# Kernel tuning notes

Measured on AMD Instinct MI355X. Metric: run time of the kernel, lower is better.

Reference implementation:

```python
import jax, jax.numpy as jnp
import numpy as np


def _gcn_norm(edge_index, num_nodes):
    # GCNConv default: add self-loops, symmetric normalization D^-1/2 (A+I) D^-1/2
    src, dst = edge_index[0], edge_index[1]
    loop = jnp.arange(num_nodes, dtype=edge_index.dtype)
    src = jnp.concatenate([src, loop])
    dst = jnp.concatenate([dst, loop])
    deg = jax.ops.segment_sum(jnp.ones_like(dst, dtype=jnp.float32), dst,
                              num_segments=num_nodes)
    dinv = jnp.where(deg > 0, jax.lax.rsqrt(deg), 0.0)
    norm = dinv[src] * dinv[dst]  # [E + N]
    return src, dst, norm


def _gcn_conv(x, W, b, src, dst, norm, num_nodes):
    # x: [B, N, Fin] -> [B, N, Fout]
    h = jnp.einsum('bnf,fh->bnh', x, W)
    msg = h[:, src, :] * norm[None, :, None]  # [B, E+N, Fout]
    agg = jax.vmap(lambda m: jax.ops.segment_sum(m, dst, num_segments=num_nodes))(msg)
    return agg + b


def setup_inputs() -> dict:
    key = jax.random.key(0)
    ks = jax.random.split(key, 10)
    B, N, E = 2, 20000, 320000
    Fin, H, Out = 128, 256, 1
    x = jax.random.normal(ks[0], (B, N, Fin), dtype=jnp.float32)
    edge_index = jax.random.randint(ks[1], (2, E), 0, N, dtype=jnp.int32)
    def lin(k, fan_in, shape):
        return jax.random.normal(k, shape, dtype=jnp.float32) / np.sqrt(fan_in)
    return {
        'x': x,
        'edge_index': edge_index,
        'W1': lin(ks[2], Fin, (Fin, H)), 'b1': jnp.zeros((H,), jnp.float32),
        'W2': lin(ks[3], H, (H, H)),     'b2': jnp.zeros((H,), jnp.float32),
        'W3': lin(ks[4], H, (H, H)),     'b3': jnp.zeros((H,), jnp.float32),
        'Wl': lin(ks[5], H, (H, Out)),   'bl': jnp.zeros((Out,), jnp.float32),
    }


def reference(x, edge_index, W1, b1, W2, b2, W3, b3, Wl, bl):
    N = x.shape[1]
    src, dst, norm = _gcn_norm(edge_index, N)
    h = jax.nn.relu(_gcn_conv(x, W1, b1, src, dst, norm, N))
    h = jax.nn.relu(_gcn_conv(h, W2, b2, src, dst, norm, N))
    h = jax.nn.relu(_gcn_conv(h, W3, b3, src, dst, norm, N))
    # AdaptiveAvgPool1d(1) over nodes -> mean over N, then linear head
    g = jnp.mean(h, axis=1)  # [B, H]
    return g @ Wl + bl  # [B, Out]
```

## Files before the change

kernel.cpp:

```cpp
#include <hip/hip_runtime.h>
#include <hip/hip_bf16.h>
#include <type_traits>

#define NN 20000
#define NE 320000
#define HD 256
#define NB 2
#define FIN 128
#define MP 40064
#define SB 79

typedef __attribute__((ext_vector_type(8))) short bf16x8;
typedef __attribute__((ext_vector_type(4))) float f32x4;

__device__ inline float bf2f(ushort u) {
    union { unsigned int i; float f; } c; c.i = ((unsigned int)u) << 16; return c.f;
}
__device__ inline ushort f2bf(float f) {
    __hip_bfloat16 h = __float2bfloat16(f);
    return *reinterpret_cast<ushort*>(&h);
}

__global__ __launch_bounds__(256) void count_kernel(const int* __restrict__ dst, int* cnt) {
    int e = blockIdx.x * 256 + threadIdx.x;
    if (e < NE) atomicAdd(&cnt[dst[e]], 1);
}

__global__ __launch_bounds__(256) void scan_blk_kernel(const int* __restrict__ cnt,
                                                       int* __restrict__ bsum,
                                                       float* __restrict__ dinv) {
    __shared__ int s[256];
    int t = threadIdx.x, b = blockIdx.x;
    int n = b * 256 + t;
    int c = (n < NN) ? cnt[n] : 0;
    if (n < NN) dinv[n] = rsqrtf(1.0f + (float)c);
    s[t] = c;
    __syncthreads();
    for (int off = 128; off; off >>= 1) {
        if (t < off) s[t] += s[t + off];
        __syncthreads();
    }
    if (t == 0) bsum[b] = s[0];
}

__global__ __launch_bounds__(256) void scan_fin_kernel(const int* __restrict__ bsum,
                                                       int* __restrict__ cnt,
                                                       int* __restrict__ rstart) {
    __shared__ int sb[128];
    __shared__ int s[256];
    int t = threadIdx.x, b = blockIdx.x;
    if (t < 128) sb[t] = (t < SB) ? bsum[t] : 0;
    __syncthreads();
    for (int off = 1; off < 128; off <<= 1) {
        int v = (t < 128 && t >= off) ? sb[t - off] : 0;
        __syncthreads();
        if (t < 128) sb[t] += v;
        __syncthreads();
    }
    int boff = (b == 0) ? 0 : sb[b - 1];
    int n = b * 256 + t;
    int c = (n < NN) ? cnt[n] : 0;
    s[t] = c;
    __syncthreads();
    for (int off = 1; off < 256; off <<= 1) {
        int v = (t >= off) ? s[t - off] : 0;
        __syncthreads();
        s[t] += v;
        __syncthreads();
    }
    int excl = s[t] - c + boff;
    if (n < NN) { rstart[n] = excl; cnt[n] = excl; }
    if (b == 0 && t == 0) rstart[NN] = NE;
}

__global__ __launch_bounds__(256) void bucket_kernel(const int* __restrict__ src,
                                                     const int* __restrict__ dst,
                                                     int* cursor, int2* edge2,
                                                     const float* __restrict__ dinv) {
    int e = blockIdx.x * 256 + threadIdx.x;
    if (e >= NE) return;
    int s = src[e], d = dst[e];
    int pos = atomicAdd(&cursor[d], 1);
    float w = dinv[s] * dinv[d];
    edge2[pos] = make_int2(s, __float_as_int(w));
}

__global__ __launch_bounds__(256) void prep_kernel(const float* __restrict__ x,
                                                   ushort* __restrict__ xb,
                                                   int* cnt, double* pool,
                                                   const float* __restrict__ W1,
                                                   const float* __restrict__ W2,
                                                   const float* __restrict__ W3,
                                                   ushort* __restrict__ w1t,
                                                   ushort* __restrict__ w2t,
                                                   ushort* __restrict__ w3t) {
    int bid = blockIdx.x;
    int t = threadIdx.x;
    if (bid < 5000) {
        int i = bid * 256 + t;
        if (i < NN) cnt[i] = 0;
        if (i < NB * HD) pool[i] = 0.0;
        size_t g = (size_t)i * 4;
        int b = (i >= (NN * FIN / 4));
        size_t rem = g - (size_t)b * NN * FIN;
        int n = (int)(rem >> 7);
        int f = (int)(rem & (FIN - 1));
        float4 v = *(const float4*)&x[g];
        ushort4 o;
        o.x = f2bf(v.x); o.y = f2bf(v.y); o.z = f2bf(v.z); o.w = f2bf(v.w);
        *(ushort4*)&xb[((size_t)n * NB + b) * FIN + f] = o;
    } else {
        const float* W; ushort* WT; int K; int i;
        if (bid < 5128)      { W = W1; WT = w1t; K = FIN; i = (bid - 5000) * 256 + t; }
        else if (bid < 5384) { W = W2; WT = w2t; K = HD;  i = (bid - 5128) * 256 + t; }
        else                 { W = W3; WT = w3t; K = HD;  i = (bid - 5384) * 256 + t; }
        int k = i >> 8, n = i & 255;
        WT[n * K + k] = f2bf(W[i]);
    }
}

template <int K>
__global__ __launch_bounds__(512, 4) void fused_kernel(const ushort* __restrict__ h,
                                                       const ushort* __restrict__ BT,
                                                       const float* __restrict__ bias,
                                                       const int2* __restrict__ edge2,
                                                       const int* __restrict__ rstart,
                                                       const float* __restrict__ dinv,
                                                       ushort* __restrict__ C) {
    constexpr int RW = NB * K;
    constexpr int EL = RW / 64;
    constexpr int NU = EL / 2;
    using VecT = std::conditional_t<EL == 8, uint4, uint2>;
    union UV { VecT v; unsigned int u[NU]; };

    __shared__ ushort As[64 * K];
    __shared__ ushort Bs[256 * 64];

    int t = threadIdx.x;
    int w = t >> 6, l = t & 63;
    int n0 = blockIdx.x * 32;
    const ushort* hb = h + l * EL;

    for (int mi = 0; mi < 4; ++mi) {
        int mloc = w * 4 + mi;
        int n = n0 + mloc;
        float acc[EL];
#pragma unroll
        for (int k = 0; k < EL; ++k) acc[k] = 0.0f;

        if (n < NN) {
            float dn = dinv[n];
            {
                UV s; s.v = *(const VecT*)&hb[(size_t)n * RW];
                float ws = dn * dn;
#pragma unroll
                for (int k = 0; k < NU; ++k) {
                    acc[2 * k]     += ws * bf2f((ushort)(s.u[k] & 0xffff));
                    acc[2 * k + 1] += ws * bf2f((ushort)(s.u[k] >> 16));
                }
            }
            int e0 = rstart[n], e1 = rstart[n + 1];
            int deg = e1 - e0;
            const int2* ep = edge2 + e0;
            int2 mt[12];
            UV r[8];
#pragma unroll
            for (int i = 0; i < 12; ++i) if (i < deg) mt[i] = ep[i];
#pragma unroll
            for (int i = 0; i < 8; ++i) if (i < deg) r[i].v = *(const VecT*)&hb[(size_t)mt[i].x * RW];

            int e = 0;
            for (; e + 4 <= deg; e += 4) {
#pragma unroll
                for (int i = 0; i < 4; ++i) {
                    float ww = __int_as_float(mt[i].y);
#pragma unroll
                    for (int k = 0; k < NU; ++k) {
                        acc[2 * k]     += ww * bf2f((ushort)(r[i].u[k] & 0xffff));
                        acc[2 * k + 1] += ww * bf2f((ushort)(r[i].u[k] >> 16));
                    }
                }
#pragma unroll
                for (int i = 0; i < 8; ++i) mt[i] = mt[i + 4];
#pragma unroll
                for (int i = 0; i < 4; ++i) r[i] = r[i + 4];
#pragma unroll
                for (int i = 0; i < 4; ++i) if (e + 12 + i < deg) mt[8 + i] = ep[e + 12 + i];
#pragma unroll
                for (int i = 4; i < 8; ++i) if (e + 4 + i < deg) r[i].v = *(const VecT*)&hb[(size_t)mt[i].x * RW];
            }
#pragma unroll
            for (int i = 0; i < 3; ++i) {
                if (e + i < deg) {
                    float ww = __int_as_float(mt[i].y);
#pragma unroll
                    for (int k = 0; k < NU; ++k) {
                        acc[2 * k]     += ww * bf2f((ushort)(r[i].u[k] & 0xffff));
                        acc[2 * k + 1] += ww * bf2f((ushort)(r[i].u[k] >> 16));
                    }
                }
            }
        }

        int arow = 2 * mloc + (l >> 5);
        if constexpr (EL == 8) {
            UV o;
#pragma unroll
            for (int k = 0; k < NU; ++k)
                o.u[k] = (unsigned int)f2bf(acc[2 * k]) | ((unsigned int)f2bf(acc[2 * k + 1]) << 16);
            *(uint4*)&As[arow * K + (((l & 31) ^ (arow & 7)) << 3)] = o.v;
        } else {
            UV o;
#pragma unroll
            for (int k = 0; k < NU; ++k)
                o.u[k] = (unsigned int)f2bf(acc[2 * k]) | ((unsigned int)f2bf(acc[2 * k + 1]) << 16);
            *(uint2*)&As[arow * K + ((((l & 31) >> 1) ^ (arow & 7)) << 3) + (l & 1) * 4] = o.v;
        }
    }

    int wr = w >> 2, wc = w & 3;
    f32x4 acc2[2][4] = {};
    constexpr int NKT = K / 64;
    for (int kt = 0; kt < NKT; ++kt) {
        if (kt > 0) __syncthreads();
#pragma unroll
        for (int i = 0; i < 4; ++i) {
            int c = i * 512 + t;
            int row = c >> 3, kc = c & 7;
            uint4 v = *(const uint4*)&BT[(size_t)row * K + kt * 64 + kc * 8];
            *(uint4*)&Bs[row * 64 + ((kc ^ (row & 7)) << 3)] = v;
        }
        __syncthreads();
#pragma unroll
        for (int s = 0; s < 2; ++s) {
            bf16x8 af[2], bfr[4];
#pragma unroll
            for (int m = 0; m < 2; ++m) {
                int row = wr * 32 + m * 16 + (l & 15);
                int chunk = kt * 8 + s * 4 + (l >> 4);
                af[m] = *(const bf16x8*)&As[row * K + ((chunk ^ (row & 7)) << 3)];
            }
#pragma unroll
            for (int nn = 0; nn < 4; ++nn) {
                int row = wc * 64 + nn * 16 + (l & 15);
                int chunk = s * 4 + (l >> 4);
                bfr[nn] = *(const bf16x8*)&Bs[row * 64 + ((chunk ^ (row & 7)) << 3)];
            }
#pragma unroll
            for (int m = 0; m < 2; ++m)
#pragma unroll
                for (int nn = 0; nn < 4; ++nn)
                    acc2[m][nn] = __builtin_amdgcn_mfma_f32_16x16x32_bf16(af[m], bfr[nn], acc2[m][nn], 0, 0, 0);
        }
    }

    size_t bm = (size_t)blockIdx.x * 64;
#pragma unroll
    for (int m = 0; m < 2; ++m) {
#pragma unroll
        for (int nn = 0; nn < 4; ++nn) {
            int col = wc * 64 + nn * 16 + (l & 15);
            float bv = bias[col];
#pragma unroll
            for (int j = 0; j < 4; ++j) {
                size_t row = bm + wr * 32 + m * 16 + (l >> 4) * 4 + j;
                float v = fmaxf(acc2[m][nn][j] + bv, 0.0f);
                C[row * HD + col] = f2bf(v);
            }
        }
    }
}

__global__ __launch_bounds__(256) void colsum_kernel(const ushort* __restrict__ h, double* pool) {
    const int NCH = 32;
    int n0 = blockIdx.x * NCH;
    int t = threadIdx.x;
    const unsigned int* hu = (const unsigned int*)h;
    int b = t >> 7;
    int f0 = (2 * t) & 255;
    float s0 = 0.0f, s1 = 0.0f;
    for (int n = n0; n < n0 + NCH; ++n) {
        unsigned int u = hu[(size_t)n * (NB * HD / 2) + t];
        s0 += bf2f((ushort)(u & 0xffff));
        s1 += bf2f((ushort)(u >> 16));
    }
    atomicAdd(&pool[b * HD + f0], (double)s0);
    atomicAdd(&pool[b * HD + f0 + 1], (double)s1);
}

__global__ __launch_bounds__(256) void head_kernel(const double* __restrict__ pool,
                                                   const float* __restrict__ Wl,
                                                   const float* __restrict__ bl,
                                                   float* __restrict__ out) {
    __shared__ double red[256];
    int f = threadIdx.x;
    for (int b = 0; b < NB; ++b) {
        double v = pool[b * HD + f] * (1.0 / NN) * (double)Wl[f];
        red[f] = v;
        __syncthreads();
        for (int off = 128; off; off >>= 1) {
            if (f < off) red[f] += red[f + off];
            __syncthreads();
        }
        if (f == 0) out[b] = (float)(red[0] + (double)bl[0]);
        __syncthreads();
    }
}

extern "C" void kernel_launch(void* const* d_in, const int* in_sizes, int n_in,
                              void* d_out, int out_size, void* d_ws, size_t ws_size,
                              hipStream_t stream) {
    const float* x  = (const float*)d_in[0];
    const int* eidx = (const int*)d_in[1];
    const float* W1 = (const float*)d_in[2];
    const float* b1 = (const float*)d_in[3];
    const float* W2 = (const float*)d_in[4];
    const float* b2 = (const float*)d_in[5];
    const float* W3 = (const float*)d_in[6];
    const float* b3 = (const float*)d_in[7];
    const float* Wl = (const float*)d_in[8];
    const float* bl = (const float*)d_in[9];
    float* out = (float*)d_out;

    const int* src = eidx;
    const int* dst = eidx + NE;

    char* p = (char*)d_ws;
    auto alloc = [&](size_t bytes) { char* r = p; p += (bytes + 255) & ~(size_t)255; return r; };
    ushort* xb    = (ushort*)alloc((size_t)MP * FIN * 2);
    ushort* bufA  = (ushort*)alloc((size_t)MP * HD * 2);
    ushort* bufB  = (ushort*)alloc((size_t)MP * HD * 2);
    ushort* w1t   = (ushort*)alloc((size_t)HD * FIN * 2);
    ushort* w2t   = (ushort*)alloc((size_t)HD * HD * 2);
    ushort* w3t   = (ushort*)alloc((size_t)HD * HD * 2);
    float*  dinv  = (float*)alloc(NN * 4);
    int2*   edge2 = (int2*)alloc((size_t)NE * 8);
    int*    cnt   = (int*)alloc(NN * 4);
    int*    rstart= (int*)alloc((NN + 1) * 4);
    int*    bsum  = (int*)alloc(SB * 4);
    double* pool  = (double*)alloc(NB * HD * 8);

    prep_kernel<<<5640, 256, 0, stream>>>(x, xb, cnt, pool, W1, W2, W3, w1t, w2t, w3t);
    count_kernel<<<(NE + 255) / 256, 256, 0, stream>>>(dst, cnt);
    scan_blk_kernel<<<SB, 256, 0, stream>>>(cnt, bsum, dinv);
    scan_fin_kernel<<<SB, 256, 0, stream>>>(bsum, cnt, rstart);
    bucket_kernel<<<(NE + 255) / 256, 256, 0, stream>>>(src, dst, cnt, edge2, dinv);

    const int FG = MP / 64;

    fused_kernel<FIN><<<FG, 512, 0, stream>>>(xb, w1t, b1, edge2, rstart, dinv, bufA);
    fused_kernel<HD><<<FG, 512, 0, stream>>>(bufA, w2t, b2, edge2, rstart, dinv, bufB);
    fused_kernel<HD><<<FG, 512, 0, stream>>>(bufB, w3t, b3, edge2, rstart, dinv, bufA);

    colsum_kernel<<<NN / 32, 256, 0, stream>>>(bufA, pool);
    head_kernel<<<1, 256, 0, stream>>>(pool, Wl, bl, out);
}
```

Before: 343.8 us.

## Shrink fused GCN blocks and read weight fragments directly from global memory

The fused aggregate+GEMM kernel moves from 512-thread blocks of 32 nodes to 256-thread blocks of 16 nodes. The shared-memory weight tile and its per-k-tile barriers are removed, so each wave loads its 64-column weight slice straight from global memory (expected to hit L2/L1). The gather prefetch depth also drops from 8 rows/12 edges to 6 rows/8 edges to cut register pressure and allow 8 blocks per CU. The cost is that weights are re-read from cache by every block with no LDS reuse, and there is less memory-level parallelism per wave in the edge gather.

```diff
diff --git a/kernel.cpp b/kernel.cpp
--- a/kernel.cpp
+++ b/kernel.cpp
@@ -120,7 +120,7 @@
 }
 
 template <int K>
-__global__ __launch_bounds__(512, 4) void fused_kernel(const ushort* __restrict__ h,
+__global__ __launch_bounds__(256, 8) void fused_kernel(const ushort* __restrict__ h,
                                                        const ushort* __restrict__ BT,
                                                        const float* __restrict__ bias,
                                                        const int2* __restrict__ edge2,
@@ -133,12 +133,11 @@
     using VecT = std::conditional_t<EL == 8, uint4, uint2>;
     union UV { VecT v; unsigned int u[NU]; };
 
-    __shared__ ushort As[64 * K];
-    __shared__ ushort Bs[256 * 64];
+    __shared__ ushort As[32 * K];
 
     int t = threadIdx.x;
     int w = t >> 6, l = t & 63;
-    int n0 = blockIdx.x * 32;
+    int n0 = blockIdx.x * 16;
     const ushort* hb = h + l * EL;
 
     for (int mi = 0; mi < 4; ++mi) {
@@ -162,89 +161,76 @@
             int e0 = rstart[n], e1 = rstart[n + 1];
             int deg = e1 - e0;
             const int2* ep = edge2 + e0;
-            int2 mt[12];
-            UV r[8];
-#pragma unroll
-            for (int i = 0; i < 12; ++i) if (i < deg) mt[i] = ep[i];
-#pragma unroll
-            for (int i = 0; i < 8; ++i) if (i < deg) r[i].v = *(const VecT*)&hb[(size_t)mt[i].x * RW];
+            int2 mt[8];
+            UV r[6];
+#pragma unroll
+            for (int i = 0; i < 8; ++i) if (i < deg) mt[i] = ep[i];
+#pragma unroll
+            for (int i = 0; i < 6; ++i) if (i < deg) r[i].v = *(const VecT*)&hb[(size_t)mt[i].x * RW];
 
             int e = 0;
-            for (; e + 4 <= deg; e += 4) {
-#pragma unroll
-                for (int i = 0; i < 4; ++i) {
-                    float ww = __int_as_float(mt[i].y);
-#pragma unroll
-                    for (int k = 0; k < NU; ++k) {
-                        acc[2 * k]     += ww * bf2f((ushort)(r[i].u[k] & 0xffff));
-                        acc[2 * k + 1] += ww * bf2f((ushort)(r[i].u[k] >> 16));
-                    }
+            for (; e + 2 <= deg; e += 2) {
+                float w0 = __int_as_float(mt[0].y);
+                float w1 = __int_as_float(mt[1].y);
+#pragma unroll
+                for (int k = 0; k < NU; ++k) {
+                    acc[2 * k]     += w0 * bf2f((ushort)(r[0].u[k] & 0xffff));
+                    acc[2 * k + 1] += w0 * bf2f((ushort)(r[0].u[k] >> 16));
                 }
 #pragma unroll
-                for (int i = 0; i < 8; ++i) mt[i] = mt[i + 4];
-#pragma unroll
-                for (int i = 0; i < 4; ++i) r[i] = r[i + 4];
-#pragma unroll
-                for (int i = 0; i < 4; ++i) if (e + 12 + i < deg) mt[8 + i] = ep[e + 12 + i];
-#pragma unroll
-                for (int i = 4; i < 8; ++i) if (e + 4 + i < deg) r[i].v = *(const VecT*)&hb[(size_t)mt[i].x * RW];
-            }
-#pragma unroll
-            for (int i = 0; i < 3; ++i) {
-                if (e + i < deg) {
-                    float ww = __int_as_float(mt[i].y);
-#pragma unroll
-                    for (int k = 0; k < NU; ++k) {
-                        acc[2 * k]     += ww * bf2f((ushort)(r[i].u[k] & 0xffff));
-                        acc[2 * k + 1] += ww * bf2f((ushort)(r[i].u[k] >> 16));
-                    }
+                for (int k = 0; k < NU; ++k) {
+                    acc[2 * k]     += w1 * bf2f((ushort)(r[1].u[k] & 0xffff));
+                    acc[2 * k + 1] += w1 * bf2f((ushort)(r[1].u[k] >> 16));
                 }
+#pragma unroll
+                for (int i = 0; i < 6; ++i) mt[i] = mt[i + 2];
+#pragma unroll
+                for (int i = 0; i < 4; ++i) r[i] = r[i + 2];
+                if (e + 8 < deg) mt[6] = ep[e + 8];
+                if (e + 9 < deg) mt[7] = ep[e + 9];
+                if (e + 6 < deg) r[4].v = *(const VecT*)&hb[(size_t)mt[4].x * RW];
+                if (e + 7 < deg) r[5].v = *(const VecT*)&hb[(size_t)mt[5].x * RW];
+            }
+            if (e < deg) {
+                float w0 = __int_as_float(mt[0].y);
+#pragma unroll
+                for (int k = 0; k < NU; ++k) {
+                    acc[2 * k]     += w0 * bf2f((ushort)(r[0].u[k] & 0xffff));
+                    acc[2 * k + 1] += w0 * bf2f((ushort)(r[0].u[k] >> 16));
+                }
             }
         }
 
         int arow = 2 * mloc + (l >> 5);
+        UV o;
+#pragma unroll
+        for (int k = 0; k < NU; ++k)
+            o.u[k] = (unsigned int)f2bf(acc[2 * k]) | ((unsigned int)f2bf(acc[2 * k + 1]) << 16);
         if constexpr (EL == 8) {
-            UV o;
-#pragma unroll
-            for (int k = 0; k < NU; ++k)
-                o.u[k] = (unsigned int)f2bf(acc[2 * k]) | ((unsigned int)f2bf(acc[2 * k + 1]) << 16);
             *(uint4*)&As[arow * K + (((l & 31) ^ (arow & 7)) << 3)] = o.v;
         } else {
-            UV o;
-#pragma unroll
-            for (int k = 0; k < NU; ++k)
-                o.u[k] = (unsigned int)f2bf(acc[2 * k]) | ((unsigned int)f2bf(acc[2 * k + 1]) << 16);
             *(uint2*)&As[arow * K + ((((l & 31) >> 1) ^ (arow & 7)) << 3) + (l & 1) * 4] = o.v;
         }
     }
-
-    int wr = w >> 2, wc = w & 3;
+    __syncthreads();
+
     f32x4 acc2[2][4] = {};
+    const ushort* Bw = BT + (size_t)(w * 64) * K;
     constexpr int NKT = K / 64;
+#pragma unroll
     for (int kt = 0; kt < NKT; ++kt) {
-        if (kt > 0) __syncthreads();
-#pragma unroll
-        for (int i = 0; i < 4; ++i) {
-            int c = i * 512 + t;
-            int row = c >> 3, kc = c & 7;
-            uint4 v = *(const uint4*)&BT[(size_t)row * K + kt * 64 + kc * 8];
-            *(uint4*)&Bs[row * 64 + ((kc ^ (row & 7)) << 3)] = v;
-        }
-        __syncthreads();
 #pragma unroll
         for (int s = 0; s < 2; ++s) {
             bf16x8 af[2], bfr[4];
 #pragma unroll
             for (int m = 0; m < 2; ++m) {
-                int row = wr * 32 + m * 16 + (l & 15);
+                int row = m * 16 + (l & 15);
                 int chunk = kt * 8 + s * 4 + (l >> 4);
                 af[m] = *(const bf16x8*)&As[row * K + ((chunk ^ (row & 7)) << 3)];
             }
 #pragma unroll
             for (int nn = 0; nn < 4; ++nn) {
-                int row = wc * 64 + nn * 16 + (l & 15);
-                int chunk = s * 4 + (l >> 4);
-                bfr[nn] = *(const bf16x8*)&Bs[row * 64 + ((chunk ^ (row & 7)) << 3)];
+                bfr[nn] = *(const bf16x8*)&Bw[(size_t)(nn * 16 + (l & 15)) * K + kt * 64 + s * 32 + (l >> 4) * 8];
             }
 #pragma unroll
             for (int m = 0; m < 2; ++m)
@@ -254,16 +240,16 @@
         }
     }
 
-    size_t bm = (size_t)blockIdx.x * 64;
+    size_t bm = (size_t)blockIdx.x * 32;
 #pragma unroll
     for (int m = 0; m < 2; ++m) {
 #pragma unroll
         for (int nn = 0; nn < 4; ++nn) {
-            int col = wc * 64 + nn * 16 + (l & 15);
+            int col = w * 64 + nn * 16 + (l & 15);
             float bv = bias[col];
 #pragma unroll
             for (int j = 0; j < 4; ++j) {
-                size_t row = bm + wr * 32 + m * 16 + (l >> 4) * 4 + j;
+                size_t row = bm + m * 16 + (l >> 4) * 4 + j;
                 float v = fmaxf(acc2[m][nn][j] + bv, 0.0f);
                 C[row * HD + col] = f2bf(v);
             }
@@ -346,11 +332,11 @@
     scan_fin_kernel<<<SB, 256, 0, stream>>>(bsum, cnt, rstart);
     bucket_kernel<<<(NE + 255) / 256, 256, 0, stream>>>(src, dst, cnt, edge2, dinv);
 
-    const int FG = MP / 64;
-
-    fused_kernel<FIN><<<FG, 512, 0, stream>>>(xb, w1t, b1, edge2, rstart, dinv, bufA);
-    fused_kernel<HD><<<FG, 512, 0, stream>>>(bufA, w2t, b2, edge2, rstart, dinv, bufB);
-    fused_kernel<HD><<<FG, 512, 0, stream>>>(bufB, w3t, b3, edge2, rstart, dinv, bufA);
+    const int FG = MP / 32;
+
+    fused_kernel<FIN><<<FG, 256, 0, stream>>>(xb, w1t, b1, edge2, rstart, dinv, bufA);
+    fused_kernel<HD><<<FG, 256, 0, stream>>>(bufA, w2t, b2, edge2, rstart, dinv, bufB);
+    fused_kernel<HD><<<FG, 256, 0, stream>>>(bufB, w3t, b3, edge2, rstart, dinv, bufA);
 
     colsum_kernel<<<NN / 32, 256, 0, stream>>>(bufA, pool);
     head_kernel<<<1, 256, 0, stream>>>(pool, Wl, bl, out);
```

Measured after the change: 691.9 us. 2.01x slower.

## Store node feature activations in FP8 to halve gather traffic

Applied to the files above, without the earlier changes.

Input features and intermediate layer activations are now stored as FP8 (e4m3 via the hardware pack/unpack builtins) instead of bf16. The edge-gather aggregation reads 4 features per 32-bit word, halving the bytes fetched per neighbour row, and the colsum kernel is rewritten to decode FP8. Weights and the MFMA path remain bf16. This cuts memory traffic in the bandwidth-bound scatter/gather but adds significant quantization error to every layer's activations, which may violate accuracy tolerance.

```diff
diff --git a/kernel.cpp b/kernel.cpp
--- a/kernel.cpp
+++ b/kernel.cpp
@@ -12,13 +12,25 @@
 
 typedef __attribute__((ext_vector_type(8))) short bf16x8;
 typedef __attribute__((ext_vector_type(4))) float f32x4;
-
-__device__ inline float bf2f(ushort u) {
-    union { unsigned int i; float f; } c; c.i = ((unsigned int)u) << 16; return c.f;
-}
+typedef __attribute__((ext_vector_type(2))) float f32x2;
+
 __device__ inline ushort f2bf(float f) {
     __hip_bfloat16 h = __float2bfloat16(f);
     return *reinterpret_cast<ushort*>(&h);
+}
+__device__ inline unsigned int pk4_fp8(float a, float b, float c, float d) {
+    int r = __builtin_amdgcn_cvt_pk_fp8_f32(a, b, 0, false);
+    r = __builtin_amdgcn_cvt_pk_fp8_f32(c, d, r, true);
+    return (unsigned int)r;
+}
+__device__ inline void acc4_fp8(float* acc, unsigned int u, float w) {
+    f32x2 lo = __builtin_amdgcn_cvt_pk_f32_fp8((int)u, false);
+    f32x2 hi = __builtin_amdgcn_cvt_pk_f32_fp8((int)u, true);
+    acc[0] += w * lo[0]; acc[1] += w * lo[1];
+    acc[2] += w * hi[0]; acc[3] += w * hi[1];
+}
+__device__ inline unsigned char f2fp8(float v) {
+    return (unsigned char)(__builtin_amdgcn_cvt_pk_fp8_f32(v, v, 0, false) & 0xff);
 }
 
 __global__ __launch_bounds__(256) void count_kernel(const int* __restrict__ dst, int* cnt) {
@@ -86,7 +98,7 @@
 }
 
 __global__ __launch_bounds__(256) void prep_kernel(const float* __restrict__ x,
-                                                   ushort* __restrict__ xb,
+                                                   unsigned int* __restrict__ xb32,
                                                    int* cnt, double* pool,
                                                    const float* __restrict__ W1,
                                                    const float* __restrict__ W2,
@@ -106,9 +118,7 @@
         int n = (int)(rem >> 7);
         int f = (int)(rem & (FIN - 1));
         float4 v = *(const float4*)&x[g];
-        ushort4 o;
-        o.x = f2bf(v.x); o.y = f2bf(v.y); o.z = f2bf(v.z); o.w = f2bf(v.w);
-        *(ushort4*)&xb[((size_t)n * NB + b) * FIN + f] = o;
+        xb32[(((size_t)n * NB + b) * FIN + f) >> 2] = pk4_fp8(v.x, v.y, v.z, v.w);
     } else {
         const float* W; ushort* WT; int K; int i;
         if (bid < 5128)      { W = W1; WT = w1t; K = FIN; i = (bid - 5000) * 256 + t; }
@@ -120,18 +130,17 @@
 }
 
 template <int K>
-__global__ __launch_bounds__(512, 4) void fused_kernel(const ushort* __restrict__ h,
+__global__ __launch_bounds__(512, 4) void fused_kernel(const unsigned char* __restrict__ h,
                                                        const ushort* __restrict__ BT,
                                                        const float* __restrict__ bias,
                                                        const int2* __restrict__ edge2,
                                                        const int* __restrict__ rstart,
                                                        const float* __restrict__ dinv,
-                                                       ushort* __restrict__ C) {
+                                                       unsigned char* __restrict__ C) {
     constexpr int RW = NB * K;
     constexpr int EL = RW / 64;
-    constexpr int NU = EL / 2;
-    using VecT = std::conditional_t<EL == 8, uint4, uint2>;
-    union UV { VecT v; unsigned int u[NU]; };
+    using VecT = std::conditional_t<EL == 8, uint2, unsigned int>;
+    union UV { VecT v; unsigned int u[EL / 4]; };
 
     __shared__ ushort As[64 * K];
     __shared__ ushort Bs[256 * 64];
@@ -139,7 +148,7 @@
     int t = threadIdx.x;
     int w = t >> 6, l = t & 63;
     int n0 = blockIdx.x * 32;
-    const ushort* hb = h + l * EL;
+    const unsigned char* hb = h + l * EL;
 
     for (int mi = 0; mi < 4; ++mi) {
         int mloc = w * 4 + mi;
@@ -154,10 +163,7 @@
                 UV s; s.v = *(const VecT*)&hb[(size_t)n * RW];
                 float ws = dn * dn;
 #pragma unroll
-                for (int k = 0; k < NU; ++k) {
-                    acc[2 * k]     += ws * bf2f((ushort)(s.u[k] & 0xffff));
-                    acc[2 * k + 1] += ws * bf2f((ushort)(s.u[k] >> 16));
-                }
+                for (int k = 0; k < EL / 4; ++k) acc4_fp8(acc + 4 * k, s.u[k], ws);
             }
             int e0 = rstart[n], e1 = rstart[n + 1];
             int deg = e1 - e0;
@@ -175,10 +181,7 @@
                 for (int i = 0; i < 4; ++i) {
                     float ww = __int_as_float(mt[i].y);
 #pragma unroll
-                    for (int k = 0; k < NU; ++k) {
-                        acc[2 * k]     += ww * bf2f((ushort)(r[i].u[k] & 0xffff));
-                        acc[2 * k + 1] += ww * bf2f((ushort)(r[i].u[k] >> 16));
-                    }
+                    for (int k = 0; k < EL / 4; ++k) acc4_fp8(acc + 4 * k, r[i].u[k], ww);
                 }
 #pragma unroll
                 for (int i = 0; i < 8; ++i) mt[i] = mt[i + 4];
@@ -194,27 +197,24 @@
                 if (e + i < deg) {
                     float ww = __int_as_float(mt[i].y);
 #pragma unroll
-                    for (int k = 0; k < NU; ++k) {
-                        acc[2 * k]     += ww * bf2f((ushort)(r[i].u[k] & 0xffff));
-                        acc[2 * k + 1] += ww * bf2f((ushort)(r[i].u[k] >> 16));
-                    }
+                    for (int k = 0; k < EL / 4; ++k) acc4_fp8(acc + 4 * k, r[i].u[k], ww);
                 }
             }
         }
 
         int arow = 2 * mloc + (l >> 5);
         if constexpr (EL == 8) {
-            UV o;
-#pragma unroll
-            for (int k = 0; k < NU; ++k)
-                o.u[k] = (unsigned int)f2bf(acc[2 * k]) | ((unsigned int)f2bf(acc[2 * k + 1]) << 16);
-            *(uint4*)&As[arow * K + (((l & 31) ^ (arow & 7)) << 3)] = o.v;
+            uint4 o;
+            o.x = (unsigned int)f2bf(acc[0]) | ((unsigned int)f2bf(acc[1]) << 16);
+            o.y = (unsigned int)f2bf(acc[2]) | ((unsigned int)f2bf(acc[3]) << 16);
+            o.z = (unsigned int)f2bf(acc[4]) | ((unsigned int)f2bf(acc[5]) << 16);
+            o.w = (unsigned int)f2bf(acc[6]) | ((unsigned int)f2bf(acc[7]) << 16);
+            *(uint4*)&As[arow * K + (((l & 31) ^ (arow & 7)) << 3)] = o;
         } else {
-            UV o;
-#pragma unroll
-            for (int k = 0; k < NU; ++k)
-                o.u[k] = (unsigned int)f2bf(acc[2 * k]) | ((unsigned int)f2bf(acc[2 * k + 1]) << 16);
-            *(uint2*)&As[arow * K + ((((l & 31) >> 1) ^ (arow & 7)) << 3) + (l & 1) * 4] = o.v;
+            uint2 o;
+            o.x = (unsigned int)f2bf(acc[0]) | ((unsigned int)f2bf(acc[1]) << 16);
+            o.y = (unsigned int)f2bf(acc[2]) | ((unsigned int)f2bf(acc[3]) << 16);
+            *(uint2*)&As[arow * K + ((((l & 31) >> 1) ^ (arow & 7)) << 3) + (l & 1) * 4] = o;
         }
     }
 
@@ -265,27 +265,31 @@
             for (int j = 0; j < 4; ++j) {
                 size_t row = bm + wr * 32 + m * 16 + (l >> 4) * 4 + j;
                 float v = fmaxf(acc2[m][nn][j] + bv, 0.0f);
-                C[row * HD + col] = f2bf(v);
-            }
-        }
-    }
-}
-
-__global__ __launch_bounds__(256) void colsum_kernel(const ushort* __restrict__ h, double* pool) {
+                C[row * HD + col] = f2fp8(v);
+            }
+        }
+    }
+}
+
+__global__ __launch_bounds__(256) void colsum_kernel(const unsigned char* __restrict__ h, double* pool) {
     const int NCH = 32;
     int n0 = blockIdx.x * NCH;
     int t = threadIdx.x;
     const unsigned int* hu = (const unsigned int*)h;
-    int b = t >> 7;
-    int f0 = (2 * t) & 255;
-    float s0 = 0.0f, s1 = 0.0f;
-    for (int n = n0; n < n0 + NCH; ++n) {
-        unsigned int u = hu[(size_t)n * (NB * HD / 2) + t];
-        s0 += bf2f((ushort)(u & 0xffff));
-        s1 += bf2f((ushort)(u >> 16));
-    }
-    atomicAdd(&pool[b * HD + f0], (double)s0);
-    atomicAdd(&pool[b * HD + f0 + 1], (double)s1);
+    int u = t & 127;
+    int b = u >> 6;
+    int f0 = (u & 63) * 4;
+    float s[4] = {0.f, 0.f, 0.f, 0.f};
+    for (int i = 0; i < NCH / 2; ++i) {
+        int n = n0 + 2 * i + (t >> 7);
+        unsigned int v = hu[(size_t)n * 128 + u];
+        f32x2 lo = __builtin_amdgcn_cvt_pk_f32_fp8((int)v, false);
+        f32x2 hi = __builtin_amdgcn_cvt_pk_f32_fp8((int)v, true);
+        s[0] += lo[0]; s[1] += lo[1]; s[2] += hi[0]; s[3] += hi[1];
+    }
+#pragma unroll
+    for (int q = 0; q < 4; ++q)
+        atomicAdd(&pool[b * HD + f0 + q], (double)s[q]);
 }
 
 __global__ __launch_bounds__(256) void head_kernel(const double* __restrict__ pool,
@@ -327,9 +331,9 @@
 
     char* p = (char*)d_ws;
     auto alloc = [&](size_t bytes) { char* r = p; p += (bytes + 255) & ~(size_t)255; return r; };
-    ushort* xb    = (ushort*)alloc((size_t)MP * FIN * 2);
-    ushort* bufA  = (ushort*)alloc((size_t)MP * HD * 2);
-    ushort* bufB  = (ushort*)alloc((size_t)MP * HD * 2);
+    unsigned char* xb   = (unsigned char*)alloc((size_t)MP * FIN);
+    unsigned char* bufA = (unsigned char*)alloc((size_t)MP * HD);
+    unsigned char* bufB = (unsigned char*)alloc((size_t)MP * HD);
     ushort* w1t   = (ushort*)alloc((size_t)HD * FIN * 2);
     ushort* w2t   = (ushort*)alloc((size_t)HD * HD * 2);
     ushort* w3t   = (ushort*)alloc((size_t)HD * HD * 2);
@@ -340,7 +344,7 @@
     int*    bsum  = (int*)alloc(SB * 4);
     double* pool  = (double*)alloc(NB * HD * 8);
 
-    prep_kernel<<<5640, 256, 0, stream>>>(x, xb, cnt, pool, W1, W2, W3, w1t, w2t, w3t);
+    prep_kernel<<<5640, 256, 0, stream>>>(x, (unsigned int*)xb, cnt, pool, W1, W2, W3, w1t, w2t, w3t);
     count_kernel<<<(NE + 255) / 256, 256, 0, stream>>>(dst, cnt);
     scan_blk_kernel<<<SB, 256, 0, stream>>>(cnt, bsum, dinv);
     scan_fin_kernel<<<SB, 256, 0, stream>>>(bsum, cnt, rstart);
```

Result: slower. 400.2 us (+16.4%).
